# Performance work log

Hardware: AMD Instinct MI355X
Metric: run time of the kernel (lower is better)

The kernel has to match this reference:

```python
import jax, jax.numpy as jnp
import numpy as np

B_, L_, D_, N_ = 2, 2048, 512, 64

def setup_inputs() -> dict:
    key = jax.random.key(0)
    ks = jax.random.split(key, 6)
    s = 1.0 / np.sqrt(D_)
    return {
        "x": jax.random.normal(ks[0], (B_, L_, D_), dtype=jnp.float32),
        "W1": jax.random.normal(ks[1], (D_, D_), dtype=jnp.float32) * s,
        "b1": jnp.zeros((D_,), dtype=jnp.float32),
        "W2": jax.random.normal(ks[2], (D_, N_), dtype=jnp.float32) * s,
        "b2": jnp.zeros((N_,), dtype=jnp.float32),
        "W3": jax.random.normal(ks[3], (D_, N_), dtype=jnp.float32) * s,
        "b3": jnp.zeros((N_,), dtype=jnp.float32),
        "A": jax.random.normal(ks[4], (D_, N_), dtype=jnp.float32) * (1.0 / np.sqrt(N_)),
    }

def reference(x, W1, b1, W2, b2, W3, b3, A):
    # Projections (faithful to fc2/fc3/fc1 in the torch module)
    B = x @ W2 + b2                                  # (b, l, n)
    C = x @ W3 + b3                                  # (b, l, n)
    delta = jax.nn.softplus(x @ W1 + b1)             # (b, l, d)
    # Discretization
    dB = jnp.einsum('bld,bln->bldn', delta, B)       # (b, l, d, n)
    dA = jnp.exp(jnp.einsum('bld,dn->bldn', delta, A))  # (b, l, d, n)
    # h is initialized to zeros in the original forward, so the dA*h term
    # contributes exactly zero; kept for faithfulness to the source math.
    h = dA * 0.0 + x[..., None] * dB                 # (b, l, d, n)
    y = jnp.einsum('bln,bldn->bld', C, h)            # (b, l, d)
    return y
```

## Files before the change

kernel.cpp:

```cpp
#include <hip/hip_runtime.h>
#include <math.h>

#define DDIM 512

typedef _Float16 f16;
typedef _Float16 f16x4 __attribute__((ext_vector_type(4)));
typedef _Float16 f16x8 __attribute__((ext_vector_type(8)));
typedef float f32x4 __attribute__((ext_vector_type(4)));

__device__ __forceinline__ float softplusf(float v) {
    return (v > 20.0f) ? v : log1pf(__expf(v));
}

__global__ __launch_bounds__(256) void prep_w(
    const float* __restrict__ W1, const float* __restrict__ W2,
    const float* __restrict__ W3, f16* __restrict__ w1t, f16* __restrict__ w23)
{
    __shared__ __align__(16) f16 lt[32][520];
    const int tid  = threadIdx.x;
    const int wb   = blockIdx.x;
    const int wv   = tid >> 6;
    const int lane = tid & 63;
    const int q    = lane >> 4;
    const int l15  = lane & 15;

    const float* src; int srcRS, col0; f16* dst;
    if (wb < 16)      { src = W1; srcRS = DDIM; col0 = wb * 32;
                        dst = w1t + (size_t)wb * 2 * 16 * 512; }
    else if (wb < 18) { src = W2; srcRS = 64;  col0 = (wb - 16) * 32;
                        dst = w23 + (size_t)(wb - 16) * 2 * 16 * 512; }
    else              { src = W3; srcRS = 64;  col0 = (wb - 18) * 32;
                        dst = w23 + (size_t)(4 + (wb - 18) * 2) * 16 * 512; }
#pragma unroll
    for (int i = 0; i < 16; ++i) {
        int f  = tid + 256 * i;
        int k  = f >> 3;
        int c4 = (f & 7) * 4;
        float4 v = *(const float4*)(src + (size_t)k * srcRS + col0 + c4);
        lt[c4 + 0][k] = (f16)v.x; lt[c4 + 1][k] = (f16)v.y;
        lt[c4 + 2][k] = (f16)v.z; lt[c4 + 3][k] = (f16)v.w;
    }
    __syncthreads();
#pragma unroll
    for (int j = 0; j < 8; ++j) {
        int s   = wv * 8 + j;
        int ntL = s >> 4;
        int kt  = s & 15;
        f16x8 vv = *(const f16x8*)&lt[ntL * 16 + l15][kt * 32 + q * 8];
        *(f16x8*)(dst + (size_t)(ntL * 16 + kt) * 512 + lane * 8) = vv;
    }
}

__global__ __launch_bounds__(512) void fused_sy(
    const float* __restrict__ x, const f16* __restrict__ w1t,
    const f16* __restrict__ w23, const float* __restrict__ b1,
    const float* __restrict__ b2, const float* __restrict__ b3,
    float* __restrict__ y)
{
    __shared__ __align__(16) float xf[16][516];
    __shared__ __align__(16) f16  xs[16][520];
    __shared__ float sp[8][16][17];
    __shared__ float s_lds[16];

    const int tid  = threadIdx.x;
    const int wv   = tid >> 6;
    const int lane = tid & 63;
    const int q    = lane >> 4;
    const int l15  = lane & 15;
    const int tb   = blockIdx.x * 16;

#pragma unroll
    for (int it = 0; it < 4; ++it) {
        int f   = tid + 512 * it;
        int row = f >> 7;
        int c4  = (f & 127) * 4;
        float4 v = *(const float4*)(x + (size_t)(tb + row) * DDIM + c4);
        *(float4*)&xf[row][c4] = v;
        f16x4 h = {(f16)v.x, (f16)v.y, (f16)v.z, (f16)v.w};
        *(f16x4*)&xs[row][c4] = h;
    }
    __syncthreads();

    {
        const f16* wS = w23 + (size_t)wv * 16 * 512 + lane * 8;
        f32x4 aclo = (f32x4){0.f, 0.f, 0.f, 0.f};
        f32x4 achi = (f32x4){0.f, 0.f, 0.f, 0.f};
#pragma unroll
        for (int kt = 0; kt < 8; ++kt) {
            f16x8 a0 = *(const f16x8*)&xs[l15][kt * 32 + q * 8];
            f16x8 a1 = *(const f16x8*)&xs[l15][(kt + 8) * 32 + q * 8];
            f16x8 w0 = *(const f16x8*)(wS + (size_t)kt * 512);
            f16x8 w1 = *(const f16x8*)(wS + (size_t)(kt + 8) * 512);
            aclo = __builtin_amdgcn_mfma_f32_16x16x32_f16(a0, w0, aclo, 0, 0, 0);
            achi = __builtin_amdgcn_mfma_f32_16x16x32_f16(a1, w1, achi, 0, 0, 0);
        }
        float bias = (wv < 4) ? b2[wv * 16 + l15] : b3[(wv - 4) * 16 + l15];
#pragma unroll
        for (int r = 0; r < 4; ++r)
            sp[wv][q * 4 + r][l15] = aclo[r] + achi[r] + bias;
    }
    __syncthreads();

    if (tid < 256) {
        int t = tid >> 4, n16 = tid & 15;
        float v = 0.f;
#pragma unroll
        for (int g = 0; g < 4; ++g)
            v += sp[g][t][n16] * sp[4 + g][t][n16];
        v += __shfl_xor(v, 1); v += __shfl_xor(v, 2);
        v += __shfl_xor(v, 4); v += __shfl_xor(v, 8);
        if (n16 == 0) s_lds[t] = v;
    }

    f32x4 acc[4];
#pragma unroll
    for (int i = 0; i < 4; ++i) acc[i] = (f32x4){0.f, 0.f, 0.f, 0.f};
    const f16* bP = w1t + (size_t)(wv * 4) * 16 * 512 + lane * 8;
#pragma unroll
    for (int kt = 0; kt < 16; ++kt) {
        f16x8 a  = *(const f16x8*)&xs[l15][kt * 32 + q * 8];
        f16x8 f0 = *(const f16x8*)(bP + (size_t)(0 * 16 + kt) * 512);
        f16x8 f1 = *(const f16x8*)(bP + (size_t)(1 * 16 + kt) * 512);
        f16x8 f2 = *(const f16x8*)(bP + (size_t)(2 * 16 + kt) * 512);
        f16x8 f3 = *(const f16x8*)(bP + (size_t)(3 * 16 + kt) * 512);
        acc[0] = __builtin_amdgcn_mfma_f32_16x16x32_f16(a, f0, acc[0], 0, 0, 0);
        acc[1] = __builtin_amdgcn_mfma_f32_16x16x32_f16(a, f1, acc[1], 0, 0, 0);
        acc[2] = __builtin_amdgcn_mfma_f32_16x16x32_f16(a, f2, acc[2], 0, 0, 0);
        acc[3] = __builtin_amdgcn_mfma_f32_16x16x32_f16(a, f3, acc[3], 0, 0, 0);
    }
    __syncthreads();

#pragma unroll
    for (int i = 0; i < 4; ++i) {
        int d = (wv * 4 + i) * 16 + l15;
        float bb = b1[d];
#pragma unroll
        for (int r = 0; r < 4; ++r) {
            int t = q * 4 + r;
            xf[t][d] = xf[t][d] * softplusf(acc[i][r] + bb) * s_lds[t];
        }
    }
    __syncthreads();

#pragma unroll
    for (int it = 0; it < 4; ++it) {
        int f   = tid + 512 * it;
        int row = f >> 7;
        int c4  = (f & 127) * 4;
        *(float4*)(y + (size_t)(tb + row) * DDIM + c4) =
            *(const float4*)&xf[row][c4];
    }
}

extern "C" void kernel_launch(void* const* d_in, const int* in_sizes, int n_in,
                              void* d_out, int out_size, void* d_ws, size_t ws_size,
                              hipStream_t stream)
{
    (void)n_in; (void)out_size; (void)ws_size;
    const float* x  = (const float*)d_in[0];
    const float* W1 = (const float*)d_in[1];
    const float* b1 = (const float*)d_in[2];
    const float* W2 = (const float*)d_in[3];
    const float* b2 = (const float*)d_in[4];
    const float* W3 = (const float*)d_in[5];
    const float* b3 = (const float*)d_in[6];
    float* y = (float*)d_out;

    char* ws = (char*)d_ws;
    f16* w1t = (f16*)ws;
    f16* w23 = (f16*)(ws + (512 << 10));

    const int M = in_sizes[0] / DDIM;

    prep_w<<<20, 256, 0, stream>>>(W1, W2, W3, w1t, w23);
    fused_sy<<<M / 16, 512, 0, stream>>>(x, w1t, w23, b1, b2, b3, y);
}
```

Measured before the change: 93.72 us.

## Retile fused kernel to 64-row by 128-column blocks and split weight prep

The main kernel now processes 64 tokens per block and splits the 512 output columns across 4 blocks in a 2D grid, so each W1 fragment loaded from global memory is reused across four row tiles instead of one. Each block recomputes the full B/C projection and the s scalar for its 64 rows, which repeats that small GEMM 4 times across column blocks. The weight-prep kernel is also split along K into 80 smaller blocks to spread the transpose and convert work over more CUs. LDS usage per block grows to hold 64 rows of fp16 x.

Measured after the change: 94.45 us. Within noise of the previous version (+0.8%).

```diff
diff --git a/kernel.cpp b/kernel.cpp
--- a/kernel.cpp
+++ b/kernel.cpp
@@ -16,7 +16,7 @@
     const float* __restrict__ W1, const float* __restrict__ W2,
     const float* __restrict__ W3, f16* __restrict__ w1t, f16* __restrict__ w23)
 {
-    __shared__ __align__(16) f16 lt[32][520];
+    __shared__ __align__(16) f16 lt[32][136];
     const int tid  = threadIdx.x;
     const int wb   = blockIdx.x;
     const int wv   = tid >> 6;
@@ -24,30 +24,37 @@
     const int q    = lane >> 4;
     const int l15  = lane & 15;
 
-    const float* src; int srcRS, col0; f16* dst;
-    if (wb < 16)      { src = W1; srcRS = DDIM; col0 = wb * 32;
-                        dst = w1t + (size_t)wb * 2 * 16 * 512; }
-    else if (wb < 18) { src = W2; srcRS = 64;  col0 = (wb - 16) * 32;
-                        dst = w23 + (size_t)(wb - 16) * 2 * 16 * 512; }
-    else              { src = W3; srcRS = 64;  col0 = (wb - 18) * 32;
-                        dst = w23 + (size_t)(4 + (wb - 18) * 2) * 16 * 512; }
+    const float* src; int srcRS, col0, k0, kt0; f16* dst;
+    if (wb < 64) {
+        int ws = wb >> 2, kc = wb & 3;
+        src = W1; srcRS = DDIM; col0 = ws * 32; k0 = kc * 128; kt0 = kc * 4;
+        dst = w1t + (size_t)(ws * 2) * 16 * 512;
+    } else if (wb < 72) {
+        int i = wb - 64, ws = i >> 2, kc = i & 3;
+        src = W2; srcRS = 64; col0 = ws * 32; k0 = kc * 128; kt0 = kc * 4;
+        dst = w23 + (size_t)(ws * 2) * 16 * 512;
+    } else {
+        int i = wb - 72, ws = i >> 2, kc = i & 3;
+        src = W3; srcRS = 64; col0 = ws * 32; k0 = kc * 128; kt0 = kc * 4;
+        dst = w23 + (size_t)(4 + ws * 2) * 16 * 512;
+    }
 #pragma unroll
-    for (int i = 0; i < 16; ++i) {
+    for (int i = 0; i < 4; ++i) {
         int f  = tid + 256 * i;
         int k  = f >> 3;
         int c4 = (f & 7) * 4;
-        float4 v = *(const float4*)(src + (size_t)k * srcRS + col0 + c4);
+        float4 v = *(const float4*)(src + (size_t)(k0 + k) * srcRS + col0 + c4);
         lt[c4 + 0][k] = (f16)v.x; lt[c4 + 1][k] = (f16)v.y;
         lt[c4 + 2][k] = (f16)v.z; lt[c4 + 3][k] = (f16)v.w;
     }
     __syncthreads();
 #pragma unroll
-    for (int j = 0; j < 8; ++j) {
-        int s   = wv * 8 + j;
-        int ntL = s >> 4;
-        int kt  = s & 15;
-        f16x8 vv = *(const f16x8*)&lt[ntL * 16 + l15][kt * 32 + q * 8];
-        *(f16x8*)(dst + (size_t)(ntL * 16 + kt) * 512 + lane * 8) = vv;
+    for (int j = 0; j < 2; ++j) {
+        int s   = wv * 2 + j;
+        int ntL = s >> 2;
+        int ktL = s & 3;
+        f16x8 vv = *(const f16x8*)&lt[ntL * 16 + l15][ktL * 32 + q * 8];
+        *(f16x8*)(dst + (size_t)(ntL * 16 + kt0 + ktL) * 512 + lane * 8) = vv;
     }
 }
 
@@ -57,87 +64,100 @@
     const float* __restrict__ b2, const float* __restrict__ b3,
     float* __restrict__ y)
 {
-    __shared__ __align__(16) float xf[16][516];
-    __shared__ __align__(16) f16  xs[16][520];
-    __shared__ float sp[8][16][17];
-    __shared__ float s_lds[16];
+    __shared__ __align__(16) f16  xs[64][520];
+    __shared__ __align__(16) float xf[64][132];
+    __shared__ float ps[4][64];
+    __shared__ float s_lds[64];
 
     const int tid  = threadIdx.x;
     const int wv   = tid >> 6;
     const int lane = tid & 63;
     const int q    = lane >> 4;
     const int l15  = lane & 15;
-    const int tb   = blockIdx.x * 16;
+    const int cB   = blockIdx.x;
+    const int rB   = blockIdx.y;
+    const int tb   = rB * 64;
 
 #pragma unroll
-    for (int it = 0; it < 4; ++it) {
+    for (int it = 0; it < 16; ++it) {
         int f   = tid + 512 * it;
         int row = f >> 7;
         int c4  = (f & 127) * 4;
         float4 v = *(const float4*)(x + (size_t)(tb + row) * DDIM + c4);
-        *(float4*)&xf[row][c4] = v;
         f16x4 h = {(f16)v.x, (f16)v.y, (f16)v.z, (f16)v.w};
         *(f16x4*)&xs[row][c4] = h;
+        if (((f >> 5) & 3) == cB)
+            *(float4*)&xf[row][c4 - cB * 128] = v;
     }
     __syncthreads();
 
     {
-        const f16* wS = w23 + (size_t)wv * 16 * 512 + lane * 8;
-        f32x4 aclo = (f32x4){0.f, 0.f, 0.f, 0.f};
-        f32x4 achi = (f32x4){0.f, 0.f, 0.f, 0.f};
+        const int mp = wv >> 2;
+        const int nc = wv & 3;
+        const f16* wB = w23 + (size_t)(nc    ) * 16 * 512 + lane * 8;
+        const f16* wC = w23 + (size_t)(nc + 4) * 16 * 512 + lane * 8;
+        f32x4 aB0 = (f32x4){0.f,0.f,0.f,0.f}, aB1 = (f32x4){0.f,0.f,0.f,0.f};
+        f32x4 aC0 = (f32x4){0.f,0.f,0.f,0.f}, aC1 = (f32x4){0.f,0.f,0.f,0.f};
 #pragma unroll
-        for (int kt = 0; kt < 8; ++kt) {
-            f16x8 a0 = *(const f16x8*)&xs[l15][kt * 32 + q * 8];
-            f16x8 a1 = *(const f16x8*)&xs[l15][(kt + 8) * 32 + q * 8];
-            f16x8 w0 = *(const f16x8*)(wS + (size_t)kt * 512);
-            f16x8 w1 = *(const f16x8*)(wS + (size_t)(kt + 8) * 512);
-            aclo = __builtin_amdgcn_mfma_f32_16x16x32_f16(a0, w0, aclo, 0, 0, 0);
-            achi = __builtin_amdgcn_mfma_f32_16x16x32_f16(a1, w1, achi, 0, 0, 0);
+        for (int kt = 0; kt < 16; ++kt) {
+            f16x8 wBv = *(const f16x8*)(wB + (size_t)kt * 512);
+            f16x8 wCv = *(const f16x8*)(wC + (size_t)kt * 512);
+            f16x8 a0 = *(const f16x8*)&xs[(2*mp+0)*16 + l15][kt * 32 + q * 8];
+            f16x8 a1 = *(const f16x8*)&xs[(2*mp+1)*16 + l15][kt * 32 + q * 8];
+            aB0 = __builtin_amdgcn_mfma_f32_16x16x32_f16(a0, wBv, aB0, 0, 0, 0);
+            aC0 = __builtin_amdgcn_mfma_f32_16x16x32_f16(a0, wCv, aC0, 0, 0, 0);
+            aB1 = __builtin_amdgcn_mfma_f32_16x16x32_f16(a1, wBv, aB1, 0, 0, 0);
+            aC1 = __builtin_amdgcn_mfma_f32_16x16x32_f16(a1, wCv, aC1, 0, 0, 0);
         }
-        float bias = (wv < 4) ? b2[wv * 16 + l15] : b3[(wv - 4) * 16 + l15];
+        float b2v = b2[nc * 16 + l15];
+        float b3v = b3[nc * 16 + l15];
 #pragma unroll
-        for (int r = 0; r < 4; ++r)
-            sp[wv][q * 4 + r][l15] = aclo[r] + achi[r] + bias;
+        for (int r = 0; r < 4; ++r) {
+            float p0 = (aB0[r] + b2v) * (aC0[r] + b3v);
+            float p1 = (aB1[r] + b2v) * (aC1[r] + b3v);
+            p0 += __shfl_xor(p0, 1); p1 += __shfl_xor(p1, 1);
+            p0 += __shfl_xor(p0, 2); p1 += __shfl_xor(p1, 2);
+            p0 += __shfl_xor(p0, 4); p1 += __shfl_xor(p1, 4);
+            p0 += __shfl_xor(p0, 8); p1 += __shfl_xor(p1, 8);
+            if (l15 == 0) {
+                ps[nc][(2*mp+0)*16 + q*4 + r] = p0;
+                ps[nc][(2*mp+1)*16 + q*4 + r] = p1;
+            }
+        }
     }
     __syncthreads();
 
-    if (tid < 256) {
-        int t = tid >> 4, n16 = tid & 15;
-        float v = 0.f;
-#pragma unroll
-        for (int g = 0; g < 4; ++g)
-            v += sp[g][t][n16] * sp[4 + g][t][n16];
-        v += __shfl_xor(v, 1); v += __shfl_xor(v, 2);
-        v += __shfl_xor(v, 4); v += __shfl_xor(v, 8);
-        if (n16 == 0) s_lds[t] = v;
-    }
+    if (tid < 64)
+        s_lds[tid] = ps[0][tid] + ps[1][tid] + ps[2][tid] + ps[3][tid];
 
-    f32x4 acc[4];
-#pragma unroll
-    for (int i = 0; i < 4; ++i) acc[i] = (f32x4){0.f, 0.f, 0.f, 0.f};
-    const f16* bP = w1t + (size_t)(wv * 4) * 16 * 512 + lane * 8;
+    f32x4 acc0 = (f32x4){0.f,0.f,0.f,0.f}, acc1 = (f32x4){0.f,0.f,0.f,0.f};
+    f32x4 acc2 = (f32x4){0.f,0.f,0.f,0.f}, acc3 = (f32x4){0.f,0.f,0.f,0.f};
+    const f16* bP = w1t + (size_t)(cB * 8 + wv) * 16 * 512 + lane * 8;
 #pragma unroll
     for (int kt = 0; kt < 16; ++kt) {
-        f16x8 a  = *(const f16x8*)&xs[l15][kt * 32 + q * 8];
-        f16x8 f0 = *(const f16x8*)(bP + (size_t)(0 * 16 + kt) * 512);
-        f16x8 f1 = *(const f16x8*)(bP + (size_t)(1 * 16 + kt) * 512);
-        f16x8 f2 = *(const f16x8*)(bP + (size_t)(2 * 16 + kt) * 512);
-        f16x8 f3 = *(const f16x8*)(bP + (size_t)(3 * 16 + kt) * 512);
-        acc[0] = __builtin_amdgcn_mfma_f32_16x16x32_f16(a, f0, acc[0], 0, 0, 0);
-        acc[1] = __builtin_amdgcn_mfma_f32_16x16x32_f16(a, f1, acc[1], 0, 0, 0);
-        acc[2] = __builtin_amdgcn_mfma_f32_16x16x32_f16(a, f2, acc[2], 0, 0, 0);
-        acc[3] = __builtin_amdgcn_mfma_f32_16x16x32_f16(a, f3, acc[3], 0, 0, 0);
+        f16x8 b  = *(const f16x8*)(bP + (size_t)kt * 512);
+        f16x8 a0 = *(const f16x8*)&xs[ 0 + l15][kt * 32 + q * 8];
+        f16x8 a1 = *(const f16x8*)&xs[16 + l15][kt * 32 + q * 8];
+        f16x8 a2 = *(const f16x8*)&xs[32 + l15][kt * 32 + q * 8];
+        f16x8 a3 = *(const f16x8*)&xs[48 + l15][kt * 32 + q * 8];
+        acc0 = __builtin_amdgcn_mfma_f32_16x16x32_f16(a0, b, acc0, 0, 0, 0);
+        acc1 = __builtin_amdgcn_mfma_f32_16x16x32_f16(a1, b, acc1, 0, 0, 0);
+        acc2 = __builtin_amdgcn_mfma_f32_16x16x32_f16(a2, b, acc2, 0, 0, 0);
+        acc3 = __builtin_amdgcn_mfma_f32_16x16x32_f16(a3, b, acc3, 0, 0, 0);
     }
     __syncthreads();
 
-#pragma unroll
-    for (int i = 0; i < 4; ++i) {
-        int d = (wv * 4 + i) * 16 + l15;
-        float bb = b1[d];
+    {
+        const int dl = wv * 16 + l15;
+        const float bb = b1[cB * 128 + dl];
 #pragma unroll
         for (int r = 0; r < 4; ++r) {
-            int t = q * 4 + r;
-            xf[t][d] = xf[t][d] * softplusf(acc[i][r] + bb) * s_lds[t];
+            int t0 = 0*16 + q*4 + r, t1 = 1*16 + q*4 + r;
+            int t2 = 2*16 + q*4 + r, t3 = 3*16 + q*4 + r;
+            xf[t0][dl] = xf[t0][dl] * softplusf(acc0[r] + bb) * s_lds[t0];
+            xf[t1][dl] = xf[t1][dl] * softplusf(acc1[r] + bb) * s_lds[t1];
+            xf[t2][dl] = xf[t2][dl] * softplusf(acc2[r] + bb) * s_lds[t2];
+            xf[t3][dl] = xf[t3][dl] * softplusf(acc3[r] + bb) * s_lds[t3];
         }
     }
     __syncthreads();
@@ -145,9 +165,9 @@
 #pragma unroll
     for (int it = 0; it < 4; ++it) {
         int f   = tid + 512 * it;
-        int row = f >> 7;
-        int c4  = (f & 127) * 4;
-        *(float4*)(y + (size_t)(tb + row) * DDIM + c4) =
+        int row = f >> 5;
+        int c4  = (f & 31) * 4;
+        *(float4*)(y + (size_t)(tb + row) * DDIM + cB * 128 + c4) =
             *(const float4*)&xf[row][c4];
     }
 }
@@ -172,6 +192,6 @@
 
     const int M = in_sizes[0] / DDIM;
 
-    prep_w<<<20, 256, 0, stream>>>(W1, W2, W3, w1t, w23);
-    fused_sy<<<M / 16, 512, 0, stream>>>(x, w1t, w23, b1, b2, b3, y);
+    prep_w<<<80, 256, 0, stream>>>(W1, W2, W3, w1t, w23);
+    fused_sy<<<dim3(4, M / 64), 512, 0, stream>>>(x, w1t, w23, b1, b2, b3, y);
 }
```
